# Performance work log

Measured on AMD Instinct MI355X. Metric: run time of the kernel, lower is better.

## Reference

```python
import jax, jax.numpy as jnp
import numpy as np

SIDE = 9
STATE = SIDE * SIDE          # 81
NA = 5                       # stay, up, down, left, right
_MOVES = [(0, 0), (-1, 0), (1, 0), (0, -1), (0, 1)]

def _dest(s, a):
    r, c = divmod(s, SIDE)
    nr, nc = r + _MOVES[a][0], c + _MOVES[a][1]
    if 0 <= nr < SIDE and 0 <= nc < SIDE:
        return nr * SIDE + nc
    return s  # off-grid moves stay in place

# inflows[i] = all (s, a) with dest(s, a) == i; flattened as edge lists.
_src, _dst = [], []
for s in range(STATE):
    for a in range(NA):
        _src.append(s * NA + a)          # flat index into action_count[B, 81*5]
        _dst.append(_dest(s, a))
INFLOW_SRC = jnp.asarray(np.array(_src, dtype=np.int32))
INFLOW_DST = jnp.asarray(np.array(_dst, dtype=np.int32))


def setup_inputs() -> dict:
    key = jax.random.key(0)
    k1, k2, k3, k4, k5 = jax.random.split(key, 5)
    B = 131072
    obs = jax.random.uniform(k1, (B, 3 * STATE), dtype=jnp.float32)
    action_count = jax.random.uniform(k2, (B, STATE, NA), dtype=jnp.float32)
    W1 = jax.random.normal(k3, (STATE, 32), dtype=jnp.float32) * 0.1
    W2 = jax.random.normal(k4, (32, 32), dtype=jnp.float32) * 0.1
    W3 = jax.random.normal(k5, (32, 1), dtype=jnp.float32) * 0.1
    b3 = jnp.zeros((1,), dtype=jnp.float32)
    return {"obs": obs, "action_count": action_count,
            "W1": W1, "W2": W2, "W3": W3, "b3": b3}


def reference(obs, action_count, W1, W2, W3, b3):
    B = obs.shape[0]
    demand_count = obs[:, 2 * STATE:]                       # [B, 81]
    af = action_count.reshape(B, STATE * NA)                # [B, 405]
    # Vectorized replacement of the per-state gather+stack+reduce_sum loops:
    # next_state_count[b, i] = sum over (s,a) in inflows[i] of action_count[b, s, a]
    next_state_count = jnp.zeros((B, STATE), af.dtype).at[:, INFLOW_DST].add(af[:, INFLOW_SRC])
    # served_demand[b, i] = min(next_state_count[b, i], demand_count[b, i])
    served_demands = jnp.minimum(next_state_count, demand_count)
    immediate_reward = jnp.sum(served_demands, axis=1)      # [B]
    # value MLP on next_state_count (hidden dense layers have no bias)
    x = jax.nn.relu(next_state_count @ W1)
    x = jax.nn.relu(x @ W2)
    next_return = (x @ W3 + b3)[:, 0]                       # [B]
    symbolic_val = immediate_reward + next_return           # stack+reduce_sum
    return symbolic_val, immediate_reward, next_return, next_state_count
```

## Files before the change

kernel.cpp:

```cpp
#include <hip/hip_runtime.h>

#define SIDE 9
#define STATE 81
#define NA 5
#define NJ (STATE * NA)
#define H1 32
#define H2 32

struct DstTab { int v[NJ]; };
constexpr DstTab make_dst() {
    DstTab t{};
    const int dr[NA] = {0, -1, 1, 0, 0};
    const int dc[NA] = {0, 0, 0, -1, 1};
    for (int s = 0; s < STATE; ++s) {
        int r = s / SIDE, c = s % SIDE;
        for (int a = 0; a < NA; ++a) {
            int nr = r + dr[a], nc = c + dc[a];
            int d = (nr >= 0 && nr < SIDE && nc >= 0 && nc < SIDE) ? nr * SIDE + nc : s;
            t.v[s * NA + a] = d;
        }
    }
    return t;
}
constexpr DstTab DST = make_dst();

__global__ __launch_bounds__(256) void grid_vpn_kernel(
    const float* __restrict__ obs,
    const float* __restrict__ af,
    const float* __restrict__ W1,
    const float* __restrict__ W2,
    const float* __restrict__ W3,
    const float* __restrict__ b3,
    float* __restrict__ out,
    int B)
{
    int b = blockIdx.x * blockDim.x + threadIdx.x;
    if (b >= B) return;

    const float* afr = af + (size_t)b * NJ;
    float nsc[STATE];
#pragma unroll
    for (int d = 0; d < STATE; ++d) nsc[d] = 0.0f;
#pragma unroll
    for (int j = 0; j < NJ; ++j) {
        nsc[DST.v[j]] += afr[j];
    }

    const float* dem = obs + (size_t)b * (3 * STATE) + 2 * STATE;
    float ir = 0.0f;
#pragma unroll
    for (int d = 0; d < STATE; ++d) ir += fminf(nsc[d], dem[d]);

    float* nso = out + 3 * (size_t)B + (size_t)b * STATE;
#pragma unroll
    for (int d = 0; d < STATE; ++d) nso[d] = nsc[d];

    float x1[H1];
#pragma unroll
    for (int j = 0; j < H1; ++j) x1[j] = 0.0f;
#pragma unroll
    for (int d = 0; d < STATE; ++d) {
        float v = nsc[d];
#pragma unroll
        for (int j = 0; j < H1; ++j) x1[j] = fmaf(v, W1[d * H1 + j], x1[j]);
    }
#pragma unroll
    for (int j = 0; j < H1; ++j) x1[j] = fmaxf(x1[j], 0.0f);

    float x2[H2];
#pragma unroll
    for (int j = 0; j < H2; ++j) x2[j] = 0.0f;
#pragma unroll
    for (int k = 0; k < H1; ++k) {
        float v = x1[k];
#pragma unroll
        for (int j = 0; j < H2; ++j) x2[j] = fmaf(v, W2[k * H2 + j], x2[j]);
    }
#pragma unroll
    for (int j = 0; j < H2; ++j) x2[j] = fmaxf(x2[j], 0.0f);

    float nr = b3[0];
#pragma unroll
    for (int k = 0; k < H2; ++k) nr = fmaf(x2[k], W3[k], nr);

    out[b] = ir + nr;
    out[(size_t)B + b] = ir;
    out[2 * (size_t)B + b] = nr;
}

extern "C" void kernel_launch(void* const* d_in, const int* in_sizes, int n_in,
                              void* d_out, int out_size, void* d_ws, size_t ws_size,
                              hipStream_t stream) {
    const float* obs = (const float*)d_in[0];
    const float* ac  = (const float*)d_in[1];
    const float* W1  = (const float*)d_in[2];
    const float* W2  = (const float*)d_in[3];
    const float* W3  = (const float*)d_in[4];
    const float* b3  = (const float*)d_in[5];
    float* out = (float*)d_out;

    int B = in_sizes[0] / (3 * STATE);
    int block = 256;
    int grid = (B + block - 1) / block;
    hipLaunchKernelGGL(grid_vpn_kernel, dim3(grid), dim3(block), 0, stream,
                       obs, ac, W1, W2, W3, b3, out, B);
}
```

Measured before the change: 439.6 us.

## Restructure into 64-row tiles with coalesced gather via shared memory and split MLP

Each block now handles 64 batch rows. Each wavefront gathers one row at a time, with lanes indexing destination states, so the loads of action_count and demand are coalesced instead of one thread streaming a whole row. The next-state counts are staged in shared memory, stored out coalesced, and the MLP is split across the four waves, each computing 8 hidden units per row through a transposed shared buffer. This removes the strided per-thread memory access and the heavy register pressure of the earlier one-thread-per-row code. The cost is extra syncthreads and shared memory, and the code now assumes B is a multiple of 64 because it has no tail guard.

```diff
diff --git a/kernel.cpp b/kernel.cpp
--- a/kernel.cpp
+++ b/kernel.cpp
@@ -1,91 +1,135 @@
 #include <hip/hip_runtime.h>
 
-#define SIDE 9
 #define STATE 81
-#define NA 5
-#define NJ (STATE * NA)
-#define H1 32
-#define H2 32
+#define NROWS 64
+#define OBSW  243
+#define AFW   405
 
-struct DstTab { int v[NJ]; };
-constexpr DstTab make_dst() {
-    DstTab t{};
-    const int dr[NA] = {0, -1, 1, 0, 0};
-    const int dc[NA] = {0, 0, 0, -1, 1};
-    for (int s = 0; s < STATE; ++s) {
-        int r = s / SIDE, c = s % SIDE;
-        for (int a = 0; a < NA; ++a) {
-            int nr = r + dr[a], nc = c + dc[a];
-            int d = (nr >= 0 && nr < SIDE && nc >= 0 && nc < SIDE) ? nr * SIDE + nc : s;
-            t.v[s * NA + a] = d;
+__device__ __forceinline__ void srcs_for(int d, int* s) {
+    int r = d / 9;
+    int c = d - r * 9;
+    s[0] = 5 * d;
+    s[1] = (r < 8) ? 5 * (d + 9) + 1 : 5 * d + 2;
+    s[2] = (r > 0) ? 5 * (d - 9) + 2 : 5 * d + 1;
+    s[3] = (c < 8) ? 5 * (d + 1) + 3 : 5 * d + 4;
+    s[4] = (c > 0) ? 5 * (d - 1) + 4 : 5 * d + 3;
+}
+
+template <int W>
+__device__ __forceinline__ void layer1(const float* __restrict__ snsc,
+                                       float* __restrict__ x1T,
+                                       const float* __restrict__ W1, int row) {
+    float x1[8];
+#pragma unroll
+    for (int j = 0; j < 8; ++j) x1[j] = 0.f;
+#pragma unroll
+    for (int d = 0; d < STATE; ++d) {
+        float v = snsc[row * STATE + d];
+#pragma unroll
+        for (int j = 0; j < 8; ++j)
+            x1[j] = fmaf(v, W1[d * 32 + W * 8 + j], x1[j]);
+    }
+#pragma unroll
+    for (int j = 0; j < 8; ++j)
+        x1T[(W * 8 + j) * 65 + row] = fmaxf(x1[j], 0.f);
+}
+
+template <int W>
+__device__ __forceinline__ void layer2(const float* __restrict__ x1T,
+                                       float* __restrict__ x2,
+                                       const float* __restrict__ W2, int row) {
+#pragma unroll
+    for (int j = 0; j < 8; ++j) x2[j] = 0.f;
+#pragma unroll
+    for (int k = 0; k < 32; ++k) {
+        float v = x1T[k * 65 + row];
+#pragma unroll
+        for (int j = 0; j < 8; ++j)
+            x2[j] = fmaf(v, W2[k * 32 + W * 8 + j], x2[j]);
+    }
+}
+
+__global__ __launch_bounds__(256, 5) void grid_vpn_kernel(
+    const float* __restrict__ obs, const float* __restrict__ af,
+    const float* __restrict__ W1, const float* __restrict__ W2,
+    const float* __restrict__ W3, const float* __restrict__ b3,
+    float* __restrict__ out, int B)
+{
+    __shared__ float snsc[NROWS * STATE];
+    __shared__ float x1T[32 * 65];
+    __shared__ float sir[NROWS];
+
+    const int t = threadIdx.x;
+    const int lane = t & 63;
+    const int w = t >> 6;
+    const int rowblk = blockIdx.x * NROWS;
+
+    const bool has2 = lane < (STATE - 64);
+    int s0[5], s1[5];
+    srcs_for(lane, s0);
+    srcs_for(has2 ? lane + 64 : lane, s1);
+
+#pragma unroll 2
+    for (int i = 0; i < 16; ++i) {
+        const int rl = w + 4 * i;
+        const int row = rowblk + rl;
+        const float* afr = af + (size_t)row * AFW;
+        const float* dem = obs + (size_t)row * OBSW + 2 * STATE;
+
+        float acc = afr[s0[0]] + afr[s0[1]] + afr[s0[2]] + afr[s0[3]] + afr[s0[4]];
+        float m = fminf(acc, dem[lane]);
+        float acc2 = 0.f, m2 = 0.f;
+        if (has2) {
+            acc2 = afr[s1[0]] + afr[s1[1]] + afr[s1[2]] + afr[s1[3]] + afr[s1[4]];
+            m2 = fminf(acc2, dem[64 + lane]);
         }
+        snsc[rl * STATE + lane] = acc;
+        if (has2) snsc[rl * STATE + 64 + lane] = acc2;
+
+        float irv = m + m2;
+#pragma unroll
+        for (int off = 32; off; off >>= 1) irv += __shfl_xor(irv, off, 64);
+        if (lane == 0) sir[rl] = irv;
     }
-    return t;
-}
-constexpr DstTab DST = make_dst();
+    __syncthreads();
 
-__global__ __launch_bounds__(256) void grid_vpn_kernel(
-    const float* __restrict__ obs,
-    const float* __restrict__ af,
-    const float* __restrict__ W1,
-    const float* __restrict__ W2,
-    const float* __restrict__ W3,
-    const float* __restrict__ b3,
-    float* __restrict__ out,
-    int B)
-{
-    int b = blockIdx.x * blockDim.x + threadIdx.x;
-    if (b >= B) return;
-
-    const float* afr = af + (size_t)b * NJ;
-    float nsc[STATE];
+    {
+        float* onsc = out + 3 * (size_t)B + (size_t)rowblk * STATE;
 #pragma unroll
-    for (int d = 0; d < STATE; ++d) nsc[d] = 0.0f;
-#pragma unroll
-    for (int j = 0; j < NJ; ++j) {
-        nsc[DST.v[j]] += afr[j];
+        for (int k = 0; k < 20; ++k) onsc[t + 256 * k] = snsc[t + 256 * k];
+        if (t < NROWS * STATE - 256 * 20) onsc[t + 5120] = snsc[t + 5120];
     }
 
-    const float* dem = obs + (size_t)b * (3 * STATE) + 2 * STATE;
-    float ir = 0.0f;
+    const int row = lane;
+    if      (w == 0) layer1<0>(snsc, x1T, W1, row);
+    else if (w == 1) layer1<1>(snsc, x1T, W1, row);
+    else if (w == 2) layer1<2>(snsc, x1T, W1, row);
+    else             layer1<3>(snsc, x1T, W1, row);
+    __syncthreads();
+
+    float x2[8];
+    if      (w == 0) layer2<0>(x1T, x2, W2, row);
+    else if (w == 1) layer2<1>(x1T, x2, W2, row);
+    else if (w == 2) layer2<2>(x1T, x2, W2, row);
+    else             layer2<3>(x1T, x2, W2, row);
+    __syncthreads();
+
 #pragma unroll
-    for (int d = 0; d < STATE; ++d) ir += fminf(nsc[d], dem[d]);
+    for (int j = 0; j < 8; ++j)
+        x1T[(w * 8 + j) * 65 + row] = fmaxf(x2[j], 0.f);
+    __syncthreads();
 
-    float* nso = out + 3 * (size_t)B + (size_t)b * STATE;
+    if (w == 0) {
+        float nr = b3[0];
 #pragma unroll
-    for (int d = 0; d < STATE; ++d) nso[d] = nsc[d];
-
-    float x1[H1];
-#pragma unroll
-    for (int j = 0; j < H1; ++j) x1[j] = 0.0f;
-#pragma unroll
-    for (int d = 0; d < STATE; ++d) {
-        float v = nsc[d];
-#pragma unroll
-        for (int j = 0; j < H1; ++j) x1[j] = fmaf(v, W1[d * H1 + j], x1[j]);
+        for (int k = 0; k < 32; ++k)
+            nr = fmaf(x1T[k * 65 + row], W3[k], nr);
+        const float ir = sir[row];
+        const size_t b = rowblk + row;
+        out[b] = ir + nr;
+        out[(size_t)B + b] = ir;
+        out[2 * (size_t)B + b] = nr;
     }
-#pragma unroll
-    for (int j = 0; j < H1; ++j) x1[j] = fmaxf(x1[j], 0.0f);
-
-    float x2[H2];
-#pragma unroll
-    for (int j = 0; j < H2; ++j) x2[j] = 0.0f;
-#pragma unroll
-    for (int k = 0; k < H1; ++k) {
-        float v = x1[k];
-#pragma unroll
-        for (int j = 0; j < H2; ++j) x2[j] = fmaf(v, W2[k * H2 + j], x2[j]);
-    }
-#pragma unroll
-    for (int j = 0; j < H2; ++j) x2[j] = fmaxf(x2[j], 0.0f);
-
-    float nr = b3[0];
-#pragma unroll
-    for (int k = 0; k < H2; ++k) nr = fmaf(x2[k], W3[k], nr);
-
-    out[b] = ir + nr;
-    out[(size_t)B + b] = ir;
-    out[2 * (size_t)B + b] = nr;
 }
 
 extern "C" void kernel_launch(void* const* d_in, const int* in_sizes, int n_in,
@@ -99,9 +143,8 @@
     const float* b3  = (const float*)d_in[5];
     float* out = (float*)d_out;
 
-    int B = in_sizes[0] / (3 * STATE);
-    int block = 256;
-    int grid = (B + block - 1) / block;
-    hipLaunchKernelGGL(grid_vpn_kernel, dim3(grid), dim3(block), 0, stream,
+    int B = in_sizes[0] / OBSW;
+    int grid = B / NROWS;
+    hipLaunchKernelGGL(grid_vpn_kernel, dim3(grid), dim3(256), 0, stream,
                        obs, ac, W1, W2, W3, b3, out, B);
 }
```

After: 824.1 us. +87.5%, slower.
